# Performance work log

Hardware: AMD Instinct MI355X
Metric: run time of the kernel (lower is better)

The kernel has to match this reference:

```python
import jax, jax.numpy as jnp
import numpy as np

EPS = 1e-5
BOUNDARY = 1.0 - EPS
TEMP = 0.5  # temperature from init_kwargs


def _safe_sqrt(t):
    # sqrt with zero (not inf/nan) gradient at t<=0; matches the analytic clamp
    # in the original custom backward (clamp(z*beta, min=eps)).
    pos = t > 0
    return jnp.where(pos, jnp.sqrt(jnp.where(pos, t, 1.0)), 0.0)


def _poincare_sim(z):
    # z: [2N, D]. Pairwise Poincare distance computed via the matmul identity
    # ||u-v||^2 = ||u||^2 + ||v||^2 - 2 u.v instead of a (2N,2N,D) broadcast.
    raw = jnp.sum(z * z, axis=-1)                      # [2N] unclamped sq norms
    sqc = jnp.clip(raw, 0.0, BOUNDARY)                 # clamped as in forward
    sqdist = jnp.maximum(raw[:, None] + raw[None, :] - 2.0 * (z @ z.T), 0.0)
    x = sqdist / ((1.0 - sqc[:, None]) * (1.0 - sqc[None, :])) * 2.0 + 1.0
    dist = jnp.log(x + _safe_sqrt(x * x - 1.0))        # arcosh(x)
    return 1.0 / (1.0 + dist)                          # Poincare similarity


def setup_inputs() -> dict:
    key = jax.random.key(0)
    k1, k2, k3, k4 = jax.random.split(key, 4)
    N, D = 4096, 8

    def ball(kg, kr):
        g = jax.random.normal(kg, (N, D), dtype=jnp.float32)
        r = jax.random.uniform(kr, (N, 1), dtype=jnp.float32) * 0.85
        return g * r / (jnp.linalg.norm(g, axis=-1, keepdims=True) + 1e-6)

    return {"z_i": ball(k1, k2), "z_j": ball(k3, k4)}


def reference(z_i, z_j):
    N = z_i.shape[0]
    z = jnp.concatenate([z_i, z_j], axis=0)            # [2N, D]
    sim = _poincare_sim(z)                             # [2N, 2N]
    idx = jnp.arange(N)
    # diag(sim, +N) and diag(sim, -N): positive pairs
    positives = jnp.concatenate([sim[idx, idx + N], sim[idx + N, idx]])  # [2N]
    mask = 1.0 - jnp.eye(2 * N, dtype=sim.dtype)       # exclude self-similarity
    denom = jnp.sum(mask * jnp.exp(sim / TEMP), axis=1)  # [2N]
    all_losses = -(positives / TEMP - jnp.log(denom))
    return jnp.sum(all_losses) / (2 * N)
```

## Files before the change

kernel.cpp:

```cpp
#include <hip/hip_runtime.h>
#include <math.h>


#define D 8
#define QS 12
#define TWO_N 8192
#define HALF_N 4096
constexpr int BLOCK   = 256;
constexpr int JC      = 64;
constexpr int IBLOCKS = 16;
constexpr int JCHUNKS = 128;
constexpr int NBLK    = IBLOCKS * JCHUNKS;
constexpr int NSEG  = 368;
constexpr int SEG_LO = 1776;
#define BOUNDARY (1.0f - 1e-5f)
#define LN2 0.6931471805599453f

typedef float f32x2 __attribute__((ext_vector_type(2)));

__device__ __forceinline__ float frcp(float x)  { return __builtin_amdgcn_rcpf(x); }
__device__ __forceinline__ float fsqrt(float x) { return __builtin_amdgcn_sqrtf(x); }
__device__ __forceinline__ float flog2(float x) { return __builtin_amdgcn_logf(x); }
__device__ __forceinline__ f32x2 splat(float v) { return (f32x2){v, v}; }

__device__ __forceinline__ float dpp_wave_sum(float v) {
    int x;
    x = __builtin_amdgcn_update_dpp(0, __float_as_int(v), 0x111, 0xf, 0xf, false);
    v += __int_as_float(x);
    x = __builtin_amdgcn_update_dpp(0, __float_as_int(v), 0x112, 0xf, 0xf, false);
    v += __int_as_float(x);
    x = __builtin_amdgcn_update_dpp(0, __float_as_int(v), 0x114, 0xf, 0xe, false);
    v += __int_as_float(x);
    x = __builtin_amdgcn_update_dpp(0, __float_as_int(v), 0x118, 0xf, 0xc, false);
    v += __int_as_float(x);
    x = __builtin_amdgcn_update_dpp(0, __float_as_int(v), 0x142, 0xa, 0xf, false);
    v += __int_as_float(x);
    x = __builtin_amdgcn_update_dpp(0, __float_as_int(v), 0x143, 0xc, 0xf, false);
    v += __int_as_float(x);
    return v;
}

__global__ __launch_bounds__(256) void prep_kernel(
    const float* __restrict__ zi, const float* __restrict__ zj,
    float* __restrict__ q, float* __restrict__ out, float2* __restrict__ tab)
{
    const int row = blockIdx.x * 256 + threadIdx.x;
    const float* src = (row < HALF_N) ? (zi + (size_t)row * D)
                                      : (zj + (size_t)(row - HALF_N) * D);
    float4 a = *(const float4*)(src);
    float4 b = *(const float4*)(src + 4);
    float raw = a.x*a.x + a.y*a.y + a.z*a.z + a.w*a.w
              + b.x*b.x + b.y*b.y + b.z*b.z + b.w*b.w;
    float inv = frcp(1.0f - fminf(raw, BOUNDARY));
    float* dst = q + (size_t)row * QS;
    *(float4*)(dst)     = a;
    *(float4*)(dst + 4) = b;
    *(float4*)(dst + 8) = make_float4(inv, inv * raw, 0.0f, 0.0f);
    if (row == 0) out[0] = 0.0f;

    if (row < NSEG) {
        const int m0 = row + SEG_LO;
        const int m1 = m0 + 1;
        float ua_f = __uint_as_float(((unsigned)(m0 >> 4) << 23) | ((unsigned)(m0 & 15) << 19));
        float ub_f = __uint_as_float(((unsigned)(m1 >> 4) << 23) | ((unsigned)(m1 & 15) << 19));
        double ua = (double)ua_f, ub = (double)ub_f;
        double ga = exp(2.0 / (1.0 + log(1.0 + ua + sqrt(ua * (ua + 2.0)))));
        double gb = exp(2.0 / (1.0 + log(1.0 + ub + sqrt(ub * (ub + 2.0)))));
        double sl = (gb - ga) / (ub - ua);
        double ic = ga - sl * ua;
        tab[row] = make_float2((float)sl, (float)ic);
    }
}

__device__ __forceinline__ float lut1(float u, const float2* __restrict__ tab)
{
    int t = (int)(__float_as_uint(u) >> 19) - SEG_LO;
    t = (t < 0) ? 0 : t;
    t = (t > NSEG - 1) ? NSEG - 1 : t;
    float2 si = tab[t];
    return fmaf(si.x, u, si.y);
}

template<int MODE>
__device__ __forceinline__ f32x2 tile_loop(
    const float* __restrict__ q, const float2* __restrict__ stab, int jbase,
    const f32x2* __restrict__ s2, f32x2 t8, f32x2 t9, f32x2 m4,
    int irow0, int irow1)
{
    f32x2 acc = splat(0.0f);
    #pragma unroll 2
    for (int cc = 0; cc < JC; ++cc) {
        const float* qp = q + (size_t)(jbase + cc) * QS;
        float4 za = *(const float4*)(qp);
        float4 zb = *(const float4*)(qp + 4);
        float2 qc = *(const float2*)(qp + 8);

        f32x2 S = splat(0.0f);
        S = __builtin_elementwise_fma(s2[0], splat(za.x), S);
        S = __builtin_elementwise_fma(s2[1], splat(za.y), S);
        S = __builtin_elementwise_fma(s2[2], splat(za.z), S);
        S = __builtin_elementwise_fma(s2[3], splat(za.w), S);
        S = __builtin_elementwise_fma(s2[4], splat(zb.x), S);
        S = __builtin_elementwise_fma(s2[5], splat(zb.y), S);
        S = __builtin_elementwise_fma(s2[6], splat(zb.z), S);
        S = __builtin_elementwise_fma(s2[7], splat(zb.w), S);

        f32x2 A = t8 * splat(qc.x);
        A = __builtin_elementwise_fma(t9, splat(qc.y), A);

        f32x2 msel;
        if (MODE == 0) {
            msel = m4;
        } else {
            const float nm = -4.0f * qc.x;
            if (MODE == 1) {
                msel = splat(nm);
            } else {
                const int j = jbase + cc;
                msel.x = (j > irow0) ? m4.x : nm;
                msel.y = (j > irow1) ? m4.y : nm;
            }
        }
        f32x2 u = __builtin_elementwise_fma(S, msel, A);
        u = __builtin_elementwise_max(u, splat(0.0f));
        acc.x += lut1(u.x, stab);
        acc.y += lut1(u.y, stab);
    }
    return acc;
}

__global__ __launch_bounds__(BLOCK, 8) void pair_kernel(
    const float* __restrict__ q, const float2* __restrict__ gtab,
    float* __restrict__ part)
{
    __shared__ alignas(16) float2 stab[NSEG];

    const int tid   = threadIdx.x;
    const int ib    = blockIdx.x >> 7;
    const int jc    = blockIdx.x & (JCHUNKS - 1);
    const int ibase = ib * 512;
    const int jbase = jc * JC;

    if (tid < NSEG / 2)
        ((float4*)stab)[tid] = ((const float4*)gtab)[tid];

    const int irow0 = ibase + tid;
    const int irow1 = irow0 + 256;
    f32x2 s2[8], t8, t9, m4;
    {
        const float* q0 = q + (size_t)irow0 * QS;
        const float* q1 = q + (size_t)irow1 * QS;
        float4 a0 = *(const float4*)(q0), b0 = *(const float4*)(q0 + 4);
        float2 c0 = *(const float2*)(q0 + 8);
        float4 a1 = *(const float4*)(q1), b1 = *(const float4*)(q1 + 4);
        float2 c1 = *(const float2*)(q1 + 8);
        s2[0] = (f32x2){a0.x, a1.x}; s2[1] = (f32x2){a0.y, a1.y};
        s2[2] = (f32x2){a0.z, a1.z}; s2[3] = (f32x2){a0.w, a1.w};
        s2[4] = (f32x2){b0.x, b1.x}; s2[5] = (f32x2){b0.y, b1.y};
        s2[6] = (f32x2){b0.z, b1.z}; s2[7] = (f32x2){b0.w, b1.w};
        t8 = (f32x2){2.0f * c0.y, 2.0f * c1.y};
        t9 = (f32x2){2.0f * c0.x, 2.0f * c1.x};
        m4 = (f32x2){-4.0f * c0.x, -4.0f * c1.x};
    }
    __syncthreads();

    f32x2 acc;
    if (jbase >= ibase + 512)
        acc = tile_loop<0>(q, stab, jbase, s2, t8, t9, m4, irow0, irow1);
    else if (jbase + JC <= ibase)
        acc = tile_loop<1>(q, stab, jbase, s2, t8, t9, m4, irow0, irow1);
    else
        acc = tile_loop<2>(q, stab, jbase, s2, t8, t9, m4, irow0, irow1);

    part[(size_t)jc * TWO_N + irow0] = acc.x;
    part[(size_t)jc * TWO_N + irow1] = acc.y;
}

__global__ __launch_bounds__(256) void reduce_kernel(
    const float* __restrict__ zi, const float* __restrict__ zj,
    const float* __restrict__ part, const float2* __restrict__ gtab,
    float* __restrict__ out)
{
    __shared__ float swred[4];
    const int tid = threadIdx.x;
    const int i   = blockIdx.x * 256 + tid;

    float rs = 0.0f;
    {
        const float* pp = part + i;
        #pragma unroll 8
        for (int c = 0; c < JCHUNKS; ++c) rs += pp[(size_t)c * TWO_N];
    }

    const int base = (i < HALF_N) ? i : (i - HALF_N);
    const float* pa = (i < HALF_N) ? (zi + (size_t)base * D) : (zj + (size_t)base * D);
    const float* pb = (i < HALF_N) ? (zj + (size_t)base * D) : (zi + (size_t)base * D);
    float4 a0 = *(const float4*)(pa), a1 = *(const float4*)(pa + 4);
    float4 b0 = *(const float4*)(pb), b1 = *(const float4*)(pb + 4);
    float rawa = a0.x*a0.x + a0.y*a0.y + a0.z*a0.z + a0.w*a0.w
               + a1.x*a1.x + a1.y*a1.y + a1.z*a1.z + a1.w*a1.w;
    float rawb = b0.x*b0.x + b0.y*b0.y + b0.z*b0.z + b0.w*b0.w
               + b1.x*b1.x + b1.y*b1.y + b1.z*b1.z + b1.w*b1.w;
    float dot  = a0.x*b0.x + a0.y*b0.y + a0.z*b0.z + a0.w*b0.w
               + a1.x*b1.x + a1.y*b1.y + a1.z*b1.z + a1.w*b1.w;
    float sqd  = fmaxf(rawa + rawb - 2.0f * dot, 0.0f);
    float inva = frcp(1.0f - fminf(rawa, BOUNDARY));
    float invb = frcp(1.0f - fminf(rawb, BOUNDARY));
    float x    = fmaf(2.0f * sqd, inva * invb, 1.0f);
    float t    = fmaf(x, x, -1.0f);
    float s    = fsqrt(fmaxf(t, 0.0f));
    float dist = flog2(x + s) * LN2;
    float sim  = frcp(1.0f + dist);

    float cy = inva * rawa;
    float A  = (2.0f * cy) * inva;
    A = fmaf(2.0f * inva, cy, A);
    float us = fmaxf(fmaf(rawa, -4.0f * inva, A), 0.0f);
    float es = lut1(us, gtab);

    float denomv = rs - es;
    float dlog = flog2(denomv) * LN2;
    float term = -(2.0f * sim - dlog);

    float ws = dpp_wave_sum(term);
    if ((tid & 63) == 63) swred[tid >> 6] = ws;
    __syncthreads();
    if (tid == 0)
        atomicAdd(out, (swred[0] + swred[1] + swred[2] + swred[3])
                           * (1.0f / (float)TWO_N));
}

extern "C" void kernel_launch(void* const* d_in, const int* in_sizes, int n_in,
                              void* d_out, int out_size, void* d_ws, size_t ws_size,
                              hipStream_t stream) {
    const float* zi = (const float*)d_in[0];
    const float* zj = (const float*)d_in[1];

    float*  q    = (float*)d_ws;
    float2* tab  = (float2*)(q + (size_t)TWO_N * QS);
    float*  part = (float*)(tab + NSEG);

    prep_kernel<<<TWO_N / 256, 256, 0, stream>>>(zi, zj, q, (float*)d_out, tab);

    pair_kernel<<<NBLK, BLOCK, 0, stream>>>(q, tab, part);

    reduce_kernel<<<TWO_N / 256, 256, 0, stream>>>(zi, zj, part, tab, (float*)d_out);
}
```

Measured before the change: 90.69 us.

## Store exp-similarity LUT in fp16 and batch column loads with split accumulators

The piecewise-linear lookup table for exp(sim/T) now stores slope and intercept as packed fp16 pairs, which halves its LDS footprint and the global copy into shared memory. The inner pair loop loads four j-columns up front before computing, and alternates between two accumulators to shorten the dependent add chain. The fp16 table loses precision in the slope and intercept, which may shift the loss value. Converting the halves back to float adds a few instructions per lookup.

```diff
diff --git a/kernel.cpp b/kernel.cpp
--- a/kernel.cpp
+++ b/kernel.cpp
@@ -8,6 +8,7 @@
 #define HALF_N 4096
 constexpr int BLOCK   = 256;
 constexpr int JC      = 64;
+constexpr int GRP     = 4;
 constexpr int IBLOCKS = 16;
 constexpr int JCHUNKS = 128;
 constexpr int NBLK    = IBLOCKS * JCHUNKS;
@@ -16,7 +17,8 @@
 #define BOUNDARY (1.0f - 1e-5f)
 #define LN2 0.6931471805599453f
 
-typedef float f32x2 __attribute__((ext_vector_type(2)));
+typedef float    f32x2 __attribute__((ext_vector_type(2)));
+typedef _Float16 f16x2 __attribute__((ext_vector_type(2)));
 
 __device__ __forceinline__ float frcp(float x)  { return __builtin_amdgcn_rcpf(x); }
 __device__ __forceinline__ float fsqrt(float x) { return __builtin_amdgcn_sqrtf(x); }
@@ -42,7 +44,7 @@
 
 __global__ __launch_bounds__(256) void prep_kernel(
     const float* __restrict__ zi, const float* __restrict__ zj,
-    float* __restrict__ q, float* __restrict__ out, float2* __restrict__ tab)
+    float* __restrict__ q, float* __restrict__ out, f16x2* __restrict__ tabh)
 {
     const int row = blockIdx.x * 256 + threadIdx.x;
     const float* src = (row < HALF_N) ? (zi + (size_t)row * D)
@@ -68,72 +70,80 @@
         double gb = exp(2.0 / (1.0 + log(1.0 + ub + sqrt(ub * (ub + 2.0)))));
         double sl = (gb - ga) / (ub - ua);
         double ic = ga - sl * ua;
-        tab[row] = make_float2((float)sl, (float)ic);
-    }
-}
-
-__device__ __forceinline__ float lut1(float u, const float2* __restrict__ tab)
+        tabh[row] = (f16x2){(_Float16)(float)sl, (_Float16)(float)ic};
+    }
+}
+
+struct QCol { float4 a; float4 b; float2 c; };
+
+__device__ __forceinline__ float lut1(float u, const f16x2* __restrict__ tab)
 {
     int t = (int)(__float_as_uint(u) >> 19) - SEG_LO;
     t = (t < 0) ? 0 : t;
     t = (t > NSEG - 1) ? NSEG - 1 : t;
-    float2 si = tab[t];
-    return fmaf(si.x, u, si.y);
+    f16x2 si = tab[t];
+    return fmaf((float)si.x, u, (float)si.y);
 }
 
 template<int MODE>
 __device__ __forceinline__ f32x2 tile_loop(
-    const float* __restrict__ q, const float2* __restrict__ stab, int jbase,
+    const float* __restrict__ q, const f16x2* __restrict__ stab, int jbase,
     const f32x2* __restrict__ s2, f32x2 t8, f32x2 t9, f32x2 m4,
     int irow0, int irow1)
 {
-    f32x2 acc = splat(0.0f);
+    f32x2 accE = splat(0.0f), accO = splat(0.0f);
     #pragma unroll 2
-    for (int cc = 0; cc < JC; ++cc) {
-        const float* qp = q + (size_t)(jbase + cc) * QS;
-        float4 za = *(const float4*)(qp);
-        float4 zb = *(const float4*)(qp + 4);
-        float2 qc = *(const float2*)(qp + 8);
-
-        f32x2 S = splat(0.0f);
-        S = __builtin_elementwise_fma(s2[0], splat(za.x), S);
-        S = __builtin_elementwise_fma(s2[1], splat(za.y), S);
-        S = __builtin_elementwise_fma(s2[2], splat(za.z), S);
-        S = __builtin_elementwise_fma(s2[3], splat(za.w), S);
-        S = __builtin_elementwise_fma(s2[4], splat(zb.x), S);
-        S = __builtin_elementwise_fma(s2[5], splat(zb.y), S);
-        S = __builtin_elementwise_fma(s2[6], splat(zb.z), S);
-        S = __builtin_elementwise_fma(s2[7], splat(zb.w), S);
-
-        f32x2 A = t8 * splat(qc.x);
-        A = __builtin_elementwise_fma(t9, splat(qc.y), A);
-
-        f32x2 msel;
-        if (MODE == 0) {
-            msel = m4;
-        } else {
-            const float nm = -4.0f * qc.x;
-            if (MODE == 1) {
-                msel = splat(nm);
+    for (int g = 0; g < JC / GRP; ++g) {
+        QCol qg[GRP];
+        #pragma unroll
+        for (int c = 0; c < GRP; ++c) {
+            const float* qp = q + (size_t)(jbase + g * GRP + c) * QS;
+            qg[c].a = *(const float4*)(qp);
+            qg[c].b = *(const float4*)(qp + 4);
+            qg[c].c = *(const float2*)(qp + 8);
+        }
+        #pragma unroll
+        for (int c = 0; c < GRP; ++c) {
+            f32x2 S = splat(0.0f);
+            S = __builtin_elementwise_fma(s2[0], splat(qg[c].a.x), S);
+            S = __builtin_elementwise_fma(s2[1], splat(qg[c].a.y), S);
+            S = __builtin_elementwise_fma(s2[2], splat(qg[c].a.z), S);
+            S = __builtin_elementwise_fma(s2[3], splat(qg[c].a.w), S);
+            S = __builtin_elementwise_fma(s2[4], splat(qg[c].b.x), S);
+            S = __builtin_elementwise_fma(s2[5], splat(qg[c].b.y), S);
+            S = __builtin_elementwise_fma(s2[6], splat(qg[c].b.z), S);
+            S = __builtin_elementwise_fma(s2[7], splat(qg[c].b.w), S);
+
+            f32x2 A = t8 * splat(qg[c].c.x);
+            A = __builtin_elementwise_fma(t9, splat(qg[c].c.y), A);
+
+            f32x2 msel;
+            if (MODE == 0) {
+                msel = m4;
             } else {
-                const int j = jbase + cc;
-                msel.x = (j > irow0) ? m4.x : nm;
-                msel.y = (j > irow1) ? m4.y : nm;
+                const float nm = -4.0f * qg[c].c.x;
+                if (MODE == 1) {
+                    msel = splat(nm);
+                } else {
+                    const int j = jbase + g * GRP + c;
+                    msel.x = (j > irow0) ? m4.x : nm;
+                    msel.y = (j > irow1) ? m4.y : nm;
+                }
             }
+            f32x2 u = __builtin_elementwise_fma(S, msel, A);
+            u = __builtin_elementwise_max(u, splat(0.0f));
+            if (c & 1) { accO.x += lut1(u.x, stab); accO.y += lut1(u.y, stab); }
+            else       { accE.x += lut1(u.x, stab); accE.y += lut1(u.y, stab); }
         }
-        f32x2 u = __builtin_elementwise_fma(S, msel, A);
-        u = __builtin_elementwise_max(u, splat(0.0f));
-        acc.x += lut1(u.x, stab);
-        acc.y += lut1(u.y, stab);
-    }
-    return acc;
+    }
+    return accE + accO;
 }
 
 __global__ __launch_bounds__(BLOCK, 8) void pair_kernel(
-    const float* __restrict__ q, const float2* __restrict__ gtab,
+    const float* __restrict__ q, const f16x2* __restrict__ gtabh,
     float* __restrict__ part)
 {
-    __shared__ alignas(16) float2 stab[NSEG];
+    __shared__ alignas(16) f16x2 stab[NSEG];
 
     const int tid   = threadIdx.x;
     const int ib    = blockIdx.x >> 7;
@@ -141,8 +151,8 @@
     const int ibase = ib * 512;
     const int jbase = jc * JC;
 
-    if (tid < NSEG / 2)
-        ((float4*)stab)[tid] = ((const float4*)gtab)[tid];
+    if (tid < NSEG / 4)
+        ((float4*)stab)[tid] = ((const float4*)gtabh)[tid];
 
     const int irow0 = ibase + tid;
     const int irow1 = irow0 + 256;
@@ -178,7 +188,7 @@
 
 __global__ __launch_bounds__(256) void reduce_kernel(
     const float* __restrict__ zi, const float* __restrict__ zj,
-    const float* __restrict__ part, const float2* __restrict__ gtab,
+    const float* __restrict__ part, const f16x2* __restrict__ gtabh,
     float* __restrict__ out)
 {
     __shared__ float swred[4];
@@ -216,7 +226,11 @@
     float A  = (2.0f * cy) * inva;
     A = fmaf(2.0f * inva, cy, A);
     float us = fmaxf(fmaf(rawa, -4.0f * inva, A), 0.0f);
-    float es = lut1(us, gtab);
+    int tt = (int)(__float_as_uint(us) >> 19) - SEG_LO;
+    tt = (tt < 0) ? 0 : tt;
+    tt = (tt > NSEG - 1) ? NSEG - 1 : tt;
+    f16x2 sih = gtabh[tt];
+    float es = fmaf((float)sih.x, us, (float)sih.y);
 
     float denomv = rs - es;
     float dlog = flog2(denomv) * LN2;
@@ -236,13 +250,13 @@
     const float* zi = (const float*)d_in[0];
     const float* zj = (const float*)d_in[1];
 
-    float*  q    = (float*)d_ws;
-    float2* tab  = (float2*)(q + (size_t)TWO_N * QS);
-    float*  part = (float*)(tab + NSEG);
-
-    prep_kernel<<<TWO_N / 256, 256, 0, stream>>>(zi, zj, q, (float*)d_out, tab);
-
-    pair_kernel<<<NBLK, BLOCK, 0, stream>>>(q, tab, part);
-
-    reduce_kernel<<<TWO_N / 256, 256, 0, stream>>>(zi, zj, part, tab, (float*)d_out);
-}
+    float* q    = (float*)d_ws;
+    f16x2* tabh = (f16x2*)(q + (size_t)TWO_N * QS);
+    float* part = (float*)((char*)tabh + 2048);
+
+    prep_kernel<<<TWO_N / 256, 256, 0, stream>>>(zi, zj, q, (float*)d_out, tabh);
+
+    pair_kernel<<<NBLK, BLOCK, 0, stream>>>(q, tabh, part);
+
+    reduce_kernel<<<TWO_N / 256, 256, 0, stream>>>(zi, zj, part, tabh, (float*)d_out);
+}
```

Result: faster. 88.06 us (-2.9%).
